# Optimization experiments

Hardware: AMD Instinct MI355X
Metric: run time of the kernel (lower is better)

## Reference

```python
import jax, jax.numpy as jnp
import numpy as np

N_NODES = 50000
N_EDGES = 500000
F_NODE, F_EDGE, D, H, L = 7, 8, 64, 128, 3


def setup_inputs() -> dict:
    key = jax.random.key(0)
    ks = jax.random.split(key, 24)
    g = lambda k, shp, fan: jax.random.normal(k, shp, dtype=jnp.float32) * (1.0 / np.sqrt(fan))
    inp = {
        "node_features": jax.random.normal(ks[0], (N_NODES, F_NODE), dtype=jnp.float32),
        "edge_attr": jax.random.normal(ks[1], (N_EDGES, F_EDGE), dtype=jnp.float32),
        "embed_W": g(ks[2], (F_NODE, D), F_NODE),
        "embed_b": jnp.zeros((D,), jnp.float32),
        "msg_W1": g(ks[3], (L, 2 * D + F_EDGE, H), 2 * D + F_EDGE),
        "msg_b1": jnp.zeros((L, H), jnp.float32),
        "msg_W2": g(ks[4], (L, H, H), H),
        "msg_b2": jnp.zeros((L, H), jnp.float32),
        "upd_W": g(ks[5], (L, D + H, D), D + H),
        "upd_b": jnp.zeros((L, D), jnp.float32),
        "ln_g": jnp.ones((L, D), jnp.float32),
        "ln_b": jnp.zeros((L, D), jnp.float32),
        "pred_W1": g(ks[6], (2 * D + F_EDGE, H), 2 * D + F_EDGE),
        "pred_b1": jnp.zeros((H,), jnp.float32),
        "pred_W2": g(ks[7], (H, H // 2), H),
        "pred_b2": jnp.zeros((H // 2,), jnp.float32),
        "pred_W3": g(ks[8], (H // 2, 1), H // 2),
        "pred_b3": jnp.zeros((1,), jnp.float32),
        "edge_index": jax.random.randint(ks[9], (2, N_EDGES), 0, N_NODES, dtype=jnp.int32),
    }
    return inp


def _layer_norm(x, g, b, eps=1e-5):
    mu = jnp.mean(x, axis=-1, keepdims=True)
    var = jnp.mean((x - mu) ** 2, axis=-1, keepdims=True)
    return (x - mu) * jax.lax.rsqrt(var + eps) * g + b


def reference(node_features, edge_attr, embed_W, embed_b, msg_W1, msg_b1, msg_W2, msg_b2,
              upd_W, upd_b, ln_g, ln_b, pred_W1, pred_b1, pred_W2, pred_b2, pred_W3, pred_b3,
              edge_index):
    src, dst = edge_index[0], edge_index[1]
    n_nodes = node_features.shape[0]
    # node embedding (dropout = identity in eval)
    x = jax.nn.relu(node_features @ embed_W + embed_b)
    ones_e = jnp.ones((edge_attr.shape[0],), dtype=x.dtype)
    counts = jax.ops.segment_sum(ones_e, dst, num_segments=n_nodes)[:, None]  # [N,1]
    for l in range(L):
        # gather + concat -> message MLP over edges
        edge_in = jnp.concatenate([x[src], x[dst], edge_attr], axis=1)  # [E, 2D+Fe]
        h = jax.nn.relu(edge_in @ msg_W1[l] + msg_b1[l])
        messages = h @ msg_W2[l] + msg_b2[l]  # [E, H]
        # scatter-add aggregation + mean normalize
        agg = jax.ops.segment_sum(messages, dst, num_segments=n_nodes)
        agg = agg / (counts + 1e-6)
        # update MLP with residual
        upd_in = jnp.concatenate([x, agg], axis=1)  # [N, D+H]
        x = x + jax.nn.relu(upd_in @ upd_W[l] + upd_b[l])
        x = _layer_norm(x, ln_g[l], ln_b[l])
    # edge predictor
    edge_in = jnp.concatenate([x[src], x[dst], edge_attr], axis=1)
    h = jax.nn.relu(edge_in @ pred_W1 + pred_b1)
    h = jax.nn.relu(h @ pred_W2 + pred_b2)
    pred = jnp.tanh(h @ pred_W3 + pred_b3)[:, 0]  # [E]
    return pred
```

## Files before the change

kernel.cpp:

```cpp
#include <hip/hip_runtime.h>

#define NN 50000
#define NE 500000
#define NBLK ((NN + 1023) / 1024)

typedef __attribute__((ext_vector_type(8))) short bf8_t;
typedef __attribute__((ext_vector_type(4))) float f4_t;
#define MFMA16(a, b, c) __builtin_amdgcn_mfma_f32_16x16x32_bf16(a, b, c, 0, 0, 0)

__device__ __forceinline__ short f2bf(float f) {
  unsigned u = __float_as_uint(f);
  u += 0x7fffu + ((u >> 16) & 1u);
  return (short)(u >> 16);
}
__device__ __forceinline__ float bf_lo(unsigned u) { return __uint_as_float(u << 16); }
__device__ __forceinline__ float bf_hi(unsigned u) { return __uint_as_float(u & 0xffff0000u); }

__global__ __launch_bounds__(256) void k_zero_f4(float4* __restrict__ p, int n4)
{
  for (int i = blockIdx.x * 256 + threadIdx.x; i < n4; i += gridDim.x * 256)
    p[i] = make_float4(0.f, 0.f, 0.f, 0.f);
}
__global__ __launch_bounds__(256) void k_zero_i(int* __restrict__ p, int n)
{
  for (int i = blockIdx.x * 256 + threadIdx.x; i < n; i += gridDim.x * 256)
    p[i] = 0;
}

__global__ __launch_bounds__(256) void k_prep_w1(const float* __restrict__ W1,
                                                 short* __restrict__ w1f)
{
  int idx = blockIdx.x * 256 + threadIdx.x;
  if (idx >= 3 * 5 * 8 * 64 * 8) return;
  int l = idx / 20480;
  int rem = idx - l * 20480;
  int ks = rem / 4096;
  int nt = (rem >> 9) & 7;
  int lane = (rem >> 3) & 63;
  int j = rem & 7;
  int k = ks * 32 + (lane >> 4) * 8 + j;
  int n = nt * 16 + (lane & 15);
  float v = (k < 136) ? W1[(size_t)l * 136 * 128 + (size_t)k * 128 + n] : 0.f;
  w1f[idx] = f2bf(v);
}
__global__ __launch_bounds__(256) void k_prep_w2(const float* __restrict__ W2,
                                                 short* __restrict__ w2f)
{
  int idx = blockIdx.x * 256 + threadIdx.x;
  if (idx >= 3 * 4 * 8 * 64 * 8) return;
  int l = idx / 16384;
  int rem = idx - l * 16384;
  int ks = rem / 4096;
  int nt = (rem >> 9) & 7;
  int lane = (rem >> 3) & 63;
  int j = rem & 7;
  int k = ks * 32 + (lane >> 4) * 8 + j;
  int n = nt * 16 + (lane & 15);
  w2f[idx] = f2bf(W2[(size_t)l * 128 * 128 + (size_t)k * 128 + n]);
}
__global__ __launch_bounds__(256) void k_prep_wu(const float* __restrict__ Wu,
                                                 short* __restrict__ wuf)
{
  int idx = blockIdx.x * 256 + threadIdx.x;
  if (idx >= 3 * 6 * 4 * 64 * 8) return;
  int l = idx / 12288;
  int rem = idx - l * 12288;
  int ks = rem / 2048;
  int nt = (rem >> 9) & 3;
  int lane = (rem >> 3) & 63;
  int j = rem & 7;
  int k = ks * 32 + (lane >> 4) * 8 + j;
  int n = nt * 16 + (lane & 15);
  wuf[idx] = f2bf(Wu[(size_t)l * 192 * 64 + (size_t)k * 64 + n]);
}
__global__ __launch_bounds__(256) void k_prep_pw1(const float* __restrict__ W1,
                                                  short* __restrict__ wf)
{
  int idx = blockIdx.x * 256 + threadIdx.x;
  if (idx >= 5 * 8 * 64 * 8) return;
  int ks = idx / 4096;
  int nt = (idx >> 9) & 7;
  int lane = (idx >> 3) & 63;
  int j = idx & 7;
  int k = ks * 32 + (lane >> 4) * 8 + j;
  int n = nt * 16 + (lane & 15);
  float v = (k < 136) ? W1[(size_t)k * 128 + n] : 0.f;
  wf[idx] = f2bf(v);
}
__global__ __launch_bounds__(256) void k_prep_pw2(const float* __restrict__ W2,
                                                  short* __restrict__ wf)
{
  int idx = blockIdx.x * 256 + threadIdx.x;
  if (idx >= 4 * 4 * 64 * 8) return;
  int ks = idx / 2048;
  int nt = (idx >> 9) & 3;
  int lane = (idx >> 3) & 63;
  int j = idx & 7;
  int k = ks * 32 + (lane >> 4) * 8 + j;
  int n = nt * 16 + (lane & 15);
  wf[idx] = f2bf(W2[(size_t)k * 64 + n]);
}
__global__ __launch_bounds__(256) void k_prep_ea(const float* __restrict__ ea,
                                                 short* __restrict__ eab)
{
  int i = blockIdx.x * 256 + threadIdx.x;
  if (i >= NE * 2) return;
  float4 v = *(const float4*)&ea[(size_t)i * 4];
  short4 o;
  o.x = f2bf(v.x); o.y = f2bf(v.y); o.z = f2bf(v.z); o.w = f2bf(v.w);
  *(short4*)&eab[(size_t)i * 4] = o;
}

__global__ __launch_bounds__(256) void k_embed(
    const float* __restrict__ nf, const float* __restrict__ We,
    const float* __restrict__ be, float* __restrict__ x, short* __restrict__ xb)
{
  int idx = blockIdx.x * 256 + threadIdx.x;
  int n = idx >> 4, g = idx & 15;
  if (n >= NN) return;
  int j0 = g * 4;
  float4 b4 = *(const float4*)&be[j0];
  float a0 = b4.x, a1 = b4.y, a2 = b4.z, a3 = b4.w;
  #pragma unroll
  for (int k = 0; k < 7; ++k) {
    float v = nf[n * 7 + k];
    float4 w = *(const float4*)&We[k * 64 + j0];
    a0 += v * w.x; a1 += v * w.y; a2 += v * w.z; a3 += v * w.w;
  }
  a0 = fmaxf(a0, 0.f); a1 = fmaxf(a1, 0.f); a2 = fmaxf(a2, 0.f); a3 = fmaxf(a3, 0.f);
  *(float4*)&x[(size_t)n * 64 + j0] = make_float4(a0, a1, a2, a3);
  short4 o; o.x = f2bf(a0); o.y = f2bf(a1); o.z = f2bf(a2); o.w = f2bf(a3);
  *(short4*)&xb[(size_t)n * 64 + j0] = o;
}

__global__ __launch_bounds__(256) void k_hist(const int* __restrict__ dst, int* __restrict__ cnt)
{
  int e = blockIdx.x * 256 + threadIdx.x;
  if (e < NE) atomicAdd(&cnt[dst[e]], 1);
}

__global__ __launch_bounds__(1024) void k_scan1(const int* __restrict__ cnt,
                                                int* __restrict__ loc, int* __restrict__ bsum)
{
  __shared__ int ws[16];
  const int b = blockIdx.x, t = threadIdx.x;
  const int i = b * 1024 + t;
  const int ln = t & 63, wv = t >> 6;
  int v = (i < NN) ? cnt[i] : 0;
  int s = v;
  #pragma unroll
  for (int off = 1; off < 64; off <<= 1) {
    int u = __shfl_up(s, off, 64);
    if (ln >= off) s += u;
  }
  if (ln == 63) ws[wv] = s;
  __syncthreads();
  if (wv == 0) {
    int wsum = (ln < 16) ? ws[ln] : 0;
    #pragma unroll
    for (int off = 1; off < 16; off <<= 1) {
      int u = __shfl_up(wsum, off, 64);
      if (ln >= off) wsum += u;
    }
    if (ln < 16) ws[ln] = wsum;
  }
  __syncthreads();
  int woff = (wv > 0) ? ws[wv - 1] : 0;
  int incl = s + woff;
  if (i < NN) loc[i] = incl - v;
  if (t == 1023) bsum[b] = incl;
}
__global__ __launch_bounds__(64) void k_scan2(const int* __restrict__ bsum,
                                              int* __restrict__ boff)
{
  const int ln = threadIdx.x;
  int v = (ln < NBLK) ? bsum[ln] : 0;
  int s = v;
  #pragma unroll
  for (int off = 1; off < 64; off <<= 1) {
    int u = __shfl_up(s, off, 64);
    if (ln >= off) s += u;
  }
  if (ln < NBLK) boff[ln] = s - v;
}
__global__ __launch_bounds__(256) void k_scan3(const int* __restrict__ loc,
                                               const int* __restrict__ boff,
                                               int* __restrict__ cur)
{
  int i = blockIdx.x * 256 + threadIdx.x;
  if (i < NN) cur[i] = loc[i] + boff[i >> 10];
}

__global__ __launch_bounds__(256) void k_fill(
    const int* __restrict__ src, const int* __restrict__ dst,
    const short* __restrict__ eab, int* __restrict__ cur,
    int* __restrict__ dstc, int* __restrict__ srcc, short* __restrict__ eac)
{
  int e = blockIdx.x * 256 + threadIdx.x;
  if (e < 128) { dstc[NE + e] = 0; srcc[NE + e] = 0; }
  if (e < NE) {
    int d = dst[e];
    int s = atomicAdd(&cur[d], 1);
    dstc[s] = d;
    srcc[s] = src[e];
    *(bf8_t*)(eac + (size_t)s * 8) = *(const bf8_t*)(eab + (size_t)e * 8);
  }
}

__global__ __launch_bounds__(256, 4) void k_y1(
    const short* __restrict__ xb, const short* __restrict__ w1f_l,
    const float* __restrict__ b1,
    short* __restrict__ y1s, short* __restrict__ y1d)
{
  const int t = threadIdx.x;
  const int wv = t >> 6, l = t & 63;
  const int m16 = l & 15, g = l >> 4;
  const int nb = blockIdx.x * 64 + wv * 16;
  if (nb >= NN) return;
  int row = nb + m16; if (row >= NN) row = NN - 1;
  const short* xr = xb + (size_t)row * 64;
  bf8_t a0 = *(const bf8_t*)(xr + g * 8);
  bf8_t a1 = *(const bf8_t*)(xr + 32 + g * 8);
  const short* wl = w1f_l + l * 8;

  f4_t accS[8], accD[8];
  #pragma unroll
  for (int nt = 0; nt < 8; ++nt) {
    float bv = b1[nt * 16 + m16];
    accS[nt] = (f4_t){0.f, 0.f, 0.f, 0.f};
    accD[nt] = (f4_t){bv, bv, bv, bv};
  }
  #pragma unroll
  for (int nt = 0; nt < 8; ++nt) {
    bf8_t b0 = *(const bf8_t*)(wl + (0 * 8 + nt) * 512);
    bf8_t b1f = *(const bf8_t*)(wl + (1 * 8 + nt) * 512);
    bf8_t b2f = *(const bf8_t*)(wl + (2 * 8 + nt) * 512);
    bf8_t b3f = *(const bf8_t*)(wl + (3 * 8 + nt) * 512);
    accS[nt] = MFMA16(a0, b0, accS[nt]);
    accS[nt] = MFMA16(a1, b1f, accS[nt]);
    accD[nt] = MFMA16(a0, b2f, accD[nt]);
    accD[nt] = MFMA16(a1, b3f, accD[nt]);
  }
  #pragma unroll
  for (int nt = 0; nt < 8; ++nt) {
    #pragma unroll
    for (int r = 0; r < 4; ++r) {
      int n = nb + g * 4 + r;
      if (n < NN) {
        y1s[(size_t)n * 128 + nt * 16 + m16] = f2bf(accS[nt][r]);
        y1d[(size_t)n * 128 + nt * 16 + m16] = f2bf(accD[nt][r]);
      }
    }
  }
}

__global__ __launch_bounds__(256, 4) void k_msg_h(
    const short* __restrict__ y1s, const short* __restrict__ y1d,
    const short* __restrict__ eac,
    const int* __restrict__ srcc, const int* __restrict__ dstc,
    const float* __restrict__ W1l,
    float* __restrict__ hagg)
{
  const int t = threadIdx.x;
  const int wv = t >> 6, ln = t & 63;
  const int p0 = blockIdx.x * 64 + wv * 16;
  if (p0 >= NE) return;

  float we[8][2];
  #pragma unroll
  for (int f = 0; f < 8; ++f) {
    we[f][0] = W1l[(128 + f) * 128 + 2 * ln];
    we[f][1] = W1l[(128 + f) * 128 + 2 * ln + 1];
  }
  const int li = ln & 15;
  int srcv = srcc[p0 + li];
  int dstv = dstc[p0 + li];
  unsigned eaw = ((const unsigned*)eac)[(size_t)(p0 + (ln >> 2)) * 4 + (ln & 3)];

  unsigned ys[16], yd[16];
  #pragma unroll
  for (int i = 0; i < 16; ++i) {
    int s = __shfl(srcv, i, 64);
    int d = __shfl(dstv, i, 64);
    ys[i] = *(const unsigned*)(y1s + (size_t)s * 128 + 2 * ln);
    yd[i] = *(const unsigned*)(y1d + (size_t)d * 128 + 2 * ln);
  }

  float s0 = 0.f, s1 = 0.f;
  int cur = -1;
  #pragma unroll
  for (int i = 0; i < 16; ++i) {
    if (p0 + i >= NE) break;
    int d = __shfl(dstv, i, 64);
    if (d != cur) {
      if (cur >= 0) {
        atomicAdd(&hagg[(size_t)cur * 128 + 2 * ln], s0);
        atomicAdd(&hagg[(size_t)cur * 128 + 2 * ln + 1], s1);
      }
      cur = d; s0 = 0.f; s1 = 0.f;
    }
    float z0 = 0.f, z1 = 0.f;
    #pragma unroll
    for (int w = 0; w < 4; ++w) {
      unsigned u = __shfl(eaw, 4 * i + w, 64);
      float e0 = bf_lo(u), e1 = bf_hi(u);
      z0 += e0 * we[2 * w][0] + e1 * we[2 * w + 1][0];
      z1 += e0 * we[2 * w][1] + e1 * we[2 * w + 1][1];
    }
    float h0 = fmaxf(bf_lo(ys[i]) + bf_lo(yd[i]) + z0, 0.f);
    float h1 = fmaxf(bf_hi(ys[i]) + bf_hi(yd[i]) + z1, 0.f);
    s0 += h0; s1 += h1;
  }
  if (cur >= 0) {
    atomicAdd(&hagg[(size_t)cur * 128 + 2 * ln], s0);
    atomicAdd(&hagg[(size_t)cur * 128 + 2 * ln + 1], s1);
  }
}

__global__ __launch_bounds__(256, 4) void k_node(
    float* __restrict__ x, short* __restrict__ xb,
    const float* __restrict__ hagg, const int* __restrict__ cnt,
    const short* __restrict__ w2f_l, const float* __restrict__ b2,
    const short* __restrict__ wuf_l, const float* __restrict__ bu,
    const float* __restrict__ lng, const float* __restrict__ lnb)
{
  __shared__ short sH[4 * 16 * 136];
  const int t = threadIdx.x;
  const int wv = t >> 6, l = t & 63;
  const int m16 = l & 15, g = l >> 4;
  const int nb = blockIdx.x * 64 + wv * 16;
  if (nb >= NN) return;
  int row = nb + m16; if (row >= NN) row = NN - 1;

  const float* hr = hagg + (size_t)row * 128;
  bf8_t a2[4];
  #pragma unroll
  for (int ks = 0; ks < 4; ++ks) {
    float4 q0 = *(const float4*)(hr + ks * 32 + g * 8);
    float4 q1 = *(const float4*)(hr + ks * 32 + g * 8 + 4);
    bf8_t av = {f2bf(q0.x), f2bf(q0.y), f2bf(q0.z), f2bf(q0.w),
                f2bf(q1.x), f2bf(q1.y), f2bf(q1.z), f2bf(q1.w)};
    a2[ks] = av;
  }
  float dg[4], iv[4];
  #pragma unroll
  for (int r = 0; r < 4; ++r) {
    int n = nb + g * 4 + r;
    int c = (n < NN) ? cnt[n] : 0;
    dg[r] = (float)c;
    iv[r] = 1.f / ((float)c + 1e-6f);
  }

  const short* w2l = w2f_l + l * 8;
  f4_t aacc[8];
  #pragma unroll
  for (int nt = 0; nt < 8; ++nt) {
    float bv = b2[nt * 16 + m16];
    aacc[nt] = (f4_t){dg[0] * bv, dg[1] * bv, dg[2] * bv, dg[3] * bv};
  }
  #pragma unroll
  for (int ks = 0; ks < 4; ++ks) {
    #pragma unroll
    for (int nt = 0; nt < 8; ++nt) {
      bf8_t bf = *(const bf8_t*)(w2l + (ks * 8 + nt) * 512);
      aacc[nt] = MFMA16(a2[ks], bf, aacc[nt]);
    }
  }

  short* sh = sH + wv * (16 * 136);
  #pragma unroll
  for (int nt = 0; nt < 8; ++nt) {
    #pragma unroll
    for (int r = 0; r < 4; ++r) {
      sh[(g * 4 + r) * 136 + nt * 16 + m16] = f2bf(aacc[nt][r] * iv[r]);
    }
  }

  const short* xr = xb + (size_t)row * 64;
  bf8_t a0 = *(const bf8_t*)(xr + g * 8);
  bf8_t a1 = *(const bf8_t*)(xr + 32 + g * 8);
  const short* wul = wuf_l + l * 8;
  f4_t acc[4];
  #pragma unroll
  for (int nt = 0; nt < 4; ++nt) {
    float bv = bu[nt * 16 + m16];
    acc[nt] = (f4_t){bv, bv, bv, bv};
  }
  #pragma unroll
  for (int nt = 0; nt < 4; ++nt) {
    acc[nt] = MFMA16(a0, *(const bf8_t*)(wul + (0 * 4 + nt) * 512), acc[nt]);
    acc[nt] = MFMA16(a1, *(const bf8_t*)(wul + (1 * 4 + nt) * 512), acc[nt]);
  }
  #pragma unroll
  for (int ks = 0; ks < 4; ++ks) {
    bf8_t af = *(const bf8_t*)(sh + m16 * 136 + ks * 32 + g * 8);
    #pragma unroll
    for (int nt = 0; nt < 4; ++nt) {
      acc[nt] = MFMA16(af, *(const bf8_t*)(wul + ((2 + ks) * 4 + nt) * 512), acc[nt]);
    }
  }

  float ov[4][4];
  #pragma unroll
  for (int nt = 0; nt < 4; ++nt) {
    #pragma unroll
    for (int r = 0; r < 4; ++r) {
      int n = nb + g * 4 + r;
      float xv = (n < NN) ? x[(size_t)n * 64 + nt * 16 + m16] : 0.f;
      ov[nt][r] = xv + fmaxf(acc[nt][r], 0.f);
    }
  }
  #pragma unroll
  for (int r = 0; r < 4; ++r) {
    float s1 = ov[0][r] + ov[1][r] + ov[2][r] + ov[3][r];
    float s2 = ov[0][r] * ov[0][r] + ov[1][r] * ov[1][r] +
               ov[2][r] * ov[2][r] + ov[3][r] * ov[3][r];
    #pragma unroll
    for (int off = 1; off < 16; off <<= 1) {
      s1 += __shfl_xor(s1, off, 64);
      s2 += __shfl_xor(s2, off, 64);
    }
    float mu = s1 * 0.015625f;
    float var = s2 * 0.015625f - mu * mu;
    float rs = rsqrtf(var + 1e-5f);
    int n = nb + g * 4 + r;
    if (n < NN) {
      #pragma unroll
      for (int nt = 0; nt < 4; ++nt) {
        int col = nt * 16 + m16;
        float y = (ov[nt][r] - mu) * rs * lng[col] + lnb[col];
        x[(size_t)n * 64 + col] = y;
        xb[(size_t)n * 64 + col] = f2bf(y);
      }
    }
  }
}

__global__ __launch_bounds__(256, 4) void k_pred2(
    const short* __restrict__ py1s, const short* __restrict__ py1d,
    const short* __restrict__ eab,
    const int* __restrict__ src, const int* __restrict__ dst,
    const float* __restrict__ pW1,
    const short* __restrict__ pw2f, const float* __restrict__ b2,
    const float* __restrict__ W3, const float* __restrict__ b3,
    float* __restrict__ out)
{
  __shared__ short sH[4 * 16 * 136];
  const int t = threadIdx.x;
  const int wv = t >> 6, ln = t & 63;
  const int m16 = ln & 15, g = ln >> 4;
  const int p0 = blockIdx.x * 64 + wv * 16;
  if (p0 >= NE) return;

  float we[8][2];
  #pragma unroll
  for (int f = 0; f < 8; ++f) {
    we[f][0] = pW1[(128 + f) * 128 + 2 * ln];
    we[f][1] = pW1[(128 + f) * 128 + 2 * ln + 1];
  }
  const int li = ln & 15;
  int ei0 = p0 + li; if (ei0 >= NE) ei0 = NE - 1;
  int srcv = src[ei0];
  int dstv = dst[ei0];
  int ee = p0 + (ln >> 2); if (ee >= NE) ee = NE - 1;
  unsigned eaw = ((const unsigned*)eab)[(size_t)ee * 4 + (ln & 3)];

  unsigned ys[16], yd[16];
  #pragma unroll
  for (int i = 0; i < 16; ++i) {
    int s = __shfl(srcv, i, 64);
    int d = __shfl(dstv, i, 64);
    ys[i] = *(const unsigned*)(py1s + (size_t)s * 128 + 2 * ln);
    yd[i] = *(const unsigned*)(py1d + (size_t)d * 128 + 2 * ln);
  }

  short* sh = sH + wv * (16 * 136);
  #pragma unroll
  for (int i = 0; i < 16; ++i) {
    float z0 = 0.f, z1 = 0.f;
    #pragma unroll
    for (int w = 0; w < 4; ++w) {
      unsigned u = __shfl(eaw, 4 * i + w, 64);
      float e0 = bf_lo(u), e1 = bf_hi(u);
      z0 += e0 * we[2 * w][0] + e1 * we[2 * w + 1][0];
      z1 += e0 * we[2 * w][1] + e1 * we[2 * w + 1][1];
    }
    float h0 = fmaxf(bf_lo(ys[i]) + bf_lo(yd[i]) + z0, 0.f);
    float h1 = fmaxf(bf_hi(ys[i]) + bf_hi(yd[i]) + z1, 0.f);
    unsigned hv = (unsigned)(unsigned short)f2bf(h0) |
                  ((unsigned)(unsigned short)f2bf(h1) << 16);
    *(unsigned*)(sh + i * 136 + 2 * ln) = hv;
  }

  f4_t acc2[4];
  #pragma unroll
  for (int nt = 0; nt < 4; ++nt) {
    float bv = b2[nt * 16 + m16];
    acc2[nt] = (f4_t){bv, bv, bv, bv};
  }
  const short* w2l = pw2f + ln * 8;
  #pragma unroll
  for (int ks = 0; ks < 4; ++ks) {
    bf8_t af = *(const bf8_t*)(sh + m16 * 136 + ks * 32 + g * 8);
    #pragma unroll
    for (int nt = 0; nt < 4; ++nt) {
      bf8_t bf = *(const bf8_t*)(w2l + (ks * 4 + nt) * 512);
      acc2[nt] = MFMA16(af, bf, acc2[nt]);
    }
  }

  float w3v[4];
  #pragma unroll
  for (int nt = 0; nt < 4; ++nt) w3v[nt] = W3[nt * 16 + m16];
  const float b3v = b3[0];
  #pragma unroll
  for (int r = 0; r < 4; ++r) {
    float v = fmaxf(acc2[0][r], 0.f) * w3v[0] + fmaxf(acc2[1][r], 0.f) * w3v[1] +
              fmaxf(acc2[2][r], 0.f) * w3v[2] + fmaxf(acc2[3][r], 0.f) * w3v[3];
    #pragma unroll
    for (int off = 1; off < 16; off <<= 1) v += __shfl_xor(v, off, 64);
    int e = p0 + g * 4 + r;
    if (m16 == 0 && e < NE) out[e] = tanhf(v + b3v);
  }
}

extern "C" void kernel_launch(void* const* d_in, const int* in_sizes, int n_in,
                              void* d_out, int out_size, void* d_ws, size_t ws_size,
                              hipStream_t stream)
{
  (void)in_sizes; (void)n_in; (void)out_size; (void)ws_size;
  const float* nf  = (const float*)d_in[0];
  const float* ea  = (const float*)d_in[1];
  const float* eW  = (const float*)d_in[2];
  const float* eb  = (const float*)d_in[3];
  const float* mW1 = (const float*)d_in[4];
  const float* mb1 = (const float*)d_in[5];
  const float* mW2 = (const float*)d_in[6];
  const float* mb2 = (const float*)d_in[7];
  const float* uW  = (const float*)d_in[8];
  const float* ub  = (const float*)d_in[9];
  const float* lg  = (const float*)d_in[10];
  const float* lb  = (const float*)d_in[11];
  const float* pW1 = (const float*)d_in[12];
  const float* pb1 = (const float*)d_in[13];
  const float* pW2 = (const float*)d_in[14];
  const float* pb2 = (const float*)d_in[15];
  const float* pW3 = (const float*)d_in[16];
  const float* pb3 = (const float*)d_in[17];
  const int*   ei  = (const int*)d_in[18];
  const int* srcI = ei;
  const int* dstI = ei + NE;
  float* out = (float*)d_out;

  char* w = (char*)d_ws;
  float* x    = (float*)w;  w += (size_t)NN * 64 * 4;
  float* hagg = (float*)w;  w += (size_t)NN * 128 * 4;
  short* xb   = (short*)w;  w += (size_t)NN * 64 * 2;
  short* eab  = (short*)w;  w += (size_t)NE * 8 * 2;
  short* eac  = (short*)w;  w += (size_t)(NE + 128) * 8 * 2;
  short* y1s  = (short*)w;  w += (size_t)NN * 128 * 2;
  short* y1d  = (short*)w;  w += (size_t)NN * 128 * 2;
  short* w1f  = (short*)w;  w += (size_t)3 * 20480 * 2;
  short* w2f  = (short*)w;  w += (size_t)3 * 16384 * 2;
  short* wuf  = (short*)w;  w += (size_t)3 * 12288 * 2;
  short* pw1f = (short*)w;  w += (size_t)20480 * 2;
  short* pw2f = (short*)w;  w += (size_t)8192 * 2;
  int*   cnt  = (int*)w;    w += (size_t)NN * 4;
  int*   loc  = (int*)w;    w += (size_t)NN * 4;
  int*   cur  = (int*)w;    w += (size_t)NN * 4;
  int*   bsum = (int*)w;    w += (size_t)64 * 4;
  int*   boff = (int*)w;    w += (size_t)64 * 4;
  int*   dstc = (int*)w;    w += (size_t)(NE + 128) * 4;
  int*   srcc = (int*)w;    w += (size_t)(NE + 128) * 4;

  k_zero_i<<<64, 256, 0, stream>>>(cnt, NN);
  k_embed<<<(NN * 16 + 255) / 256, 256, 0, stream>>>(nf, eW, eb, x, xb);
  k_hist<<<(NE + 255) / 256, 256, 0, stream>>>(dstI, cnt);
  k_scan1<<<NBLK, 1024, 0, stream>>>(cnt, loc, bsum);
  k_scan2<<<1, 64, 0, stream>>>(bsum, boff);
  k_scan3<<<(NN + 255) / 256, 256, 0, stream>>>(loc, boff, cur);
  k_prep_ea<<<(NE * 2 + 255) / 256, 256, 0, stream>>>(ea, eab);
  k_fill<<<(NE + 255) / 256, 256, 0, stream>>>(srcI, dstI, eab, cur, dstc, srcc, eac);
  k_prep_w1<<<240, 256, 0, stream>>>(mW1, w1f);
  k_prep_w2<<<192, 256, 0, stream>>>(mW2, w2f);
  k_prep_wu<<<144, 256, 0, stream>>>(uW, wuf);
  k_prep_pw1<<<80, 256, 0, stream>>>(pW1, pw1f);
  k_prep_pw2<<<32, 256, 0, stream>>>(pW2, pw2f);

  const int ngrid = (NN + 63) / 64;
  const int egrid = (NE + 63) / 64;
  for (int l = 0; l < 3; ++l) {
    k_zero_f4<<<1024, 256, 0, stream>>>((float4*)hagg, NN * 128 / 4);
    k_y1<<<ngrid, 256, 0, stream>>>(xb, w1f + (size_t)l * 20480,
        mb1 + (size_t)l * 128, y1s, y1d);
    k_msg_h<<<egrid, 256, 0, stream>>>(y1s, y1d, eac, srcc, dstc,
        mW1 + (size_t)l * 136 * 128, hagg);
    k_node<<<ngrid, 256, 0, stream>>>(x, xb, hagg, cnt,
        w2f + (size_t)l * 16384, mb2 + (size_t)l * 128,
        wuf + (size_t)l * 12288, ub + (size_t)l * 64,
        lg + (size_t)l * 64, lb + (size_t)l * 64);
  }
  k_y1<<<ngrid, 256, 0, stream>>>(xb, pw1f, pb1, y1s, y1d);
  k_pred2<<<egrid, 256, 0, stream>>>(y1s, y1d, eab, srcI, dstI,
      pW1, pw2f, pb2, pW3, pb3, out);
}
```

Measured before the change: 586.4 us.

## Replace edge-parallel atomic scatter with node-parallel CSR gather for message aggregation

The message kernel now assigns one wavefront per destination node, walks that node's CSR edge range and writes the summed hidden activations directly. This removes the per-layer zeroing of the aggregation buffer, the float atomics and the dstc array. The y1d row is loaded once per node instead of once per edge. In exchange each edge is processed serially inside the wavefront, so edge loads become dependent and load balance follows node degree, which could expose latency.

```diff
diff --git a/kernel.cpp b/kernel.cpp
--- a/kernel.cpp
+++ b/kernel.cpp
@@ -15,12 +15,10 @@
 }
 __device__ __forceinline__ float bf_lo(unsigned u) { return __uint_as_float(u << 16); }
 __device__ __forceinline__ float bf_hi(unsigned u) { return __uint_as_float(u & 0xffff0000u); }
-
-__global__ __launch_bounds__(256) void k_zero_f4(float4* __restrict__ p, int n4)
-{
-  for (int i = blockIdx.x * 256 + threadIdx.x; i < n4; i += gridDim.x * 256)
-    p[i] = make_float4(0.f, 0.f, 0.f, 0.f);
-}
+__device__ __forceinline__ float bf2f(short s) {
+  return __uint_as_float(((unsigned)(unsigned short)s) << 16);
+}
+
 __global__ __launch_bounds__(256) void k_zero_i(int* __restrict__ p, int n)
 {
   for (int i = blockIdx.x * 256 + threadIdx.x; i < n; i += gridDim.x * 256)
@@ -185,23 +183,27 @@
 }
 __global__ __launch_bounds__(256) void k_scan3(const int* __restrict__ loc,
                                                const int* __restrict__ boff,
+                                               int* __restrict__ ptr,
                                                int* __restrict__ cur)
 {
   int i = blockIdx.x * 256 + threadIdx.x;
-  if (i < NN) cur[i] = loc[i] + boff[i >> 10];
+  if (i < NN) {
+    int v = loc[i] + boff[i >> 10];
+    ptr[i] = v;
+    cur[i] = v;
+  }
 }
 
 __global__ __launch_bounds__(256) void k_fill(
     const int* __restrict__ src, const int* __restrict__ dst,
     const short* __restrict__ eab, int* __restrict__ cur,
-    int* __restrict__ dstc, int* __restrict__ srcc, short* __restrict__ eac)
+    int* __restrict__ srcc, short* __restrict__ eac)
 {
   int e = blockIdx.x * 256 + threadIdx.x;
-  if (e < 128) { dstc[NE + e] = 0; srcc[NE + e] = 0; }
+  if (e < 128) srcc[NE + e] = 0;
   if (e < NE) {
     int d = dst[e];
     int s = atomicAdd(&cur[d], 1);
-    dstc[s] = d;
     srcc[s] = src[e];
     *(bf8_t*)(eac + (size_t)s * 8) = *(const bf8_t*)(eab + (size_t)e * 8);
   }
@@ -254,17 +256,17 @@
   }
 }
 
-__global__ __launch_bounds__(256, 4) void k_msg_h(
+__global__ __launch_bounds__(256, 4) void k_msg_n(
     const short* __restrict__ y1s, const short* __restrict__ y1d,
-    const short* __restrict__ eac,
-    const int* __restrict__ srcc, const int* __restrict__ dstc,
+    const short* __restrict__ eac, const int* __restrict__ srcc,
+    const int* __restrict__ ptr, const int* __restrict__ cnt,
     const float* __restrict__ W1l,
     float* __restrict__ hagg)
 {
   const int t = threadIdx.x;
   const int wv = t >> 6, ln = t & 63;
-  const int p0 = blockIdx.x * 64 + wv * 16;
-  if (p0 >= NE) return;
+  const int n = blockIdx.x * 4 + wv;
+  if (n >= NN) return;
 
   float we[8][2];
   #pragma unroll
@@ -272,49 +274,28 @@
     we[f][0] = W1l[(128 + f) * 128 + 2 * ln];
     we[f][1] = W1l[(128 + f) * 128 + 2 * ln + 1];
   }
-  const int li = ln & 15;
-  int srcv = srcc[p0 + li];
-  int dstv = dstc[p0 + li];
-  unsigned eaw = ((const unsigned*)eac)[(size_t)(p0 + (ln >> 2)) * 4 + (ln & 3)];
-
-  unsigned ys[16], yd[16];
-  #pragma unroll
-  for (int i = 0; i < 16; ++i) {
-    int s = __shfl(srcv, i, 64);
-    int d = __shfl(dstv, i, 64);
-    ys[i] = *(const unsigned*)(y1s + (size_t)s * 128 + 2 * ln);
-    yd[i] = *(const unsigned*)(y1d + (size_t)d * 128 + 2 * ln);
-  }
+  const int p0 = ptr[n];
+  const int p1 = p0 + cnt[n];
+
+  unsigned ydu = *(const unsigned*)(y1d + (size_t)n * 128 + 2 * ln);
+  const float yd0 = bf_lo(ydu), yd1 = bf_hi(ydu);
 
   float s0 = 0.f, s1 = 0.f;
-  int cur = -1;
-  #pragma unroll
-  for (int i = 0; i < 16; ++i) {
-    if (p0 + i >= NE) break;
-    int d = __shfl(dstv, i, 64);
-    if (d != cur) {
-      if (cur >= 0) {
-        atomicAdd(&hagg[(size_t)cur * 128 + 2 * ln], s0);
-        atomicAdd(&hagg[(size_t)cur * 128 + 2 * ln + 1], s1);
-      }
-      cur = d; s0 = 0.f; s1 = 0.f;
-    }
+  for (int e = p0; e < p1; ++e) {
+    int s = srcc[e];
+    unsigned ysu = *(const unsigned*)(y1s + (size_t)s * 128 + 2 * ln);
+    bf8_t eav = *(const bf8_t*)(eac + (size_t)e * 8);
     float z0 = 0.f, z1 = 0.f;
     #pragma unroll
-    for (int w = 0; w < 4; ++w) {
-      unsigned u = __shfl(eaw, 4 * i + w, 64);
-      float e0 = bf_lo(u), e1 = bf_hi(u);
-      z0 += e0 * we[2 * w][0] + e1 * we[2 * w + 1][0];
-      z1 += e0 * we[2 * w][1] + e1 * we[2 * w + 1][1];
-    }
-    float h0 = fmaxf(bf_lo(ys[i]) + bf_lo(yd[i]) + z0, 0.f);
-    float h1 = fmaxf(bf_hi(ys[i]) + bf_hi(yd[i]) + z1, 0.f);
-    s0 += h0; s1 += h1;
-  }
-  if (cur >= 0) {
-    atomicAdd(&hagg[(size_t)cur * 128 + 2 * ln], s0);
-    atomicAdd(&hagg[(size_t)cur * 128 + 2 * ln + 1], s1);
-  }
+    for (int f = 0; f < 8; ++f) {
+      float ef = bf2f(eav[f]);
+      z0 += ef * we[f][0];
+      z1 += ef * we[f][1];
+    }
+    s0 += fmaxf(bf_lo(ysu) + yd0 + z0, 0.f);
+    s1 += fmaxf(bf_hi(ysu) + yd1 + z1, 0.f);
+  }
+  *(float2*)(hagg + (size_t)n * 128 + 2 * ln) = make_float2(s0, s1);
 }
 
 __global__ __launch_bounds__(256, 4) void k_node(
@@ -567,10 +548,10 @@
   short* pw2f = (short*)w;  w += (size_t)8192 * 2;
   int*   cnt  = (int*)w;    w += (size_t)NN * 4;
   int*   loc  = (int*)w;    w += (size_t)NN * 4;
+  int*   ptr  = (int*)w;    w += (size_t)NN * 4;
   int*   cur  = (int*)w;    w += (size_t)NN * 4;
   int*   bsum = (int*)w;    w += (size_t)64 * 4;
   int*   boff = (int*)w;    w += (size_t)64 * 4;
-  int*   dstc = (int*)w;    w += (size_t)(NE + 128) * 4;
   int*   srcc = (int*)w;    w += (size_t)(NE + 128) * 4;
 
   k_zero_i<<<64, 256, 0, stream>>>(cnt, NN);
@@ -578,9 +559,9 @@
   k_hist<<<(NE + 255) / 256, 256, 0, stream>>>(dstI, cnt);
   k_scan1<<<NBLK, 1024, 0, stream>>>(cnt, loc, bsum);
   k_scan2<<<1, 64, 0, stream>>>(bsum, boff);
-  k_scan3<<<(NN + 255) / 256, 256, 0, stream>>>(loc, boff, cur);
+  k_scan3<<<(NN + 255) / 256, 256, 0, stream>>>(loc, boff, ptr, cur);
   k_prep_ea<<<(NE * 2 + 255) / 256, 256, 0, stream>>>(ea, eab);
-  k_fill<<<(NE + 255) / 256, 256, 0, stream>>>(srcI, dstI, eab, cur, dstc, srcc, eac);
+  k_fill<<<(NE + 255) / 256, 256, 0, stream>>>(srcI, dstI, eab, cur, srcc, eac);
   k_prep_w1<<<240, 256, 0, stream>>>(mW1, w1f);
   k_prep_w2<<<192, 256, 0, stream>>>(mW2, w2f);
   k_prep_wu<<<144, 256, 0, stream>>>(uW, wuf);
@@ -589,11 +570,11 @@
 
   const int ngrid = (NN + 63) / 64;
   const int egrid = (NE + 63) / 64;
+  const int mgrid = (NN + 3) / 4;
   for (int l = 0; l < 3; ++l) {
-    k_zero_f4<<<1024, 256, 0, stream>>>((float4*)hagg, NN * 128 / 4);
     k_y1<<<ngrid, 256, 0, stream>>>(xb, w1f + (size_t)l * 20480,
         mb1 + (size_t)l * 128, y1s, y1d);
-    k_msg_h<<<egrid, 256, 0, stream>>>(y1s, y1d, eac, srcc, dstc,
+    k_msg_n<<<mgrid, 256, 0, stream>>>(y1s, y1d, eac, srcc, ptr, cnt,
         mW1 + (size_t)l * 136 * 128, hagg);
     k_node<<<ngrid, 256, 0, stream>>>(x, xb, hagg, cnt,
         w2f + (size_t)l * 16384, mb2 + (size_t)l * 128,
```

Measured after the change: 537.8 us. 1.09x faster.
